# Kernel tuning notes

Hardware: AMD Instinct MI355X
Metric: run time of the kernel (lower is better)

Reference implementation:

```python
import jax, jax.numpy as jnp
import numpy as np

GROUP_SIZE = 128
TOP_K = 2
ZERO_POINT = 8  # Marlin symmetric zero point: w = scale * (q - 8)


def _dequant_int4(q, scales, group_size):
    # q: [E, N, K] int values in [0,15]; scales: [E, N, K//group_size]
    s = jnp.repeat(scales, group_size, axis=-1)  # [E, N, K]
    return (q.astype(jnp.float32) - float(ZERO_POINT)) * s


def setup_inputs() -> dict:
    key = jax.random.key(0)
    k1, k2, k3, k4, k5, k6 = jax.random.split(key, 6)
    B, S, H, I, E = 2, 1024, 2048, 1408, 8
    router_logits = jax.random.normal(k1, (B, S, E), dtype=jnp.float32)
    hidden_states = jax.random.normal(k2, (B, S, H), dtype=jnp.float32)
    fc_gate_up_qweights = jax.random.randint(k3, (E, 2 * I, H), 0, 16, dtype=jnp.int32)
    fc_gate_up_scales = jax.random.uniform(k4, (E, 2 * I, H // GROUP_SIZE), dtype=jnp.float32) * 0.02
    fc_down_qweights = jax.random.randint(k5, (E, H, I), 0, 16, dtype=jnp.int32)
    fc_down_scales = jax.random.uniform(k6, (E, H, I // GROUP_SIZE), dtype=jnp.float32) * 0.02
    return {
        "router_logits": router_logits,
        "hidden_states": hidden_states,
        "fc_gate_up_qweights": fc_gate_up_qweights,
        "fc_gate_up_scales": fc_gate_up_scales,
        "fc_down_qweights": fc_down_qweights,
        "fc_down_scales": fc_down_scales,
    }


def reference(router_logits, hidden_states, fc_gate_up_qweights, fc_gate_up_scales,
              fc_down_qweights, fc_down_scales):
    B, S, H = hidden_states.shape
    E = router_logits.shape[-1]
    T = B * S
    x = hidden_states.reshape(T, H)
    logits = router_logits.reshape(T, E)

    # top-k routing with softmax over selected logits
    top_vals, top_idx = jax.lax.top_k(logits, TOP_K)          # [T, k]
    top_w = jax.nn.softmax(top_vals, axis=-1)                 # [T, k]
    route_w = jnp.zeros((T, E), x.dtype).at[jnp.arange(T)[:, None], top_idx].set(top_w)  # [T, E]

    # dequantize int4 weights: scale * (q - 8), per-group along K
    w_gate_up = _dequant_int4(fc_gate_up_qweights, fc_gate_up_scales, GROUP_SIZE)  # [E, 2I, H]
    w_down = _dequant_int4(fc_down_qweights, fc_down_scales, GROUP_SIZE)          # [E, H, I]

    # grouped GEMM (dense over experts, masked by routing weights)
    gu = jnp.einsum('th,enh->ten', x, w_gate_up)              # [T, E, 2I]
    gate, up = jnp.split(gu, 2, axis=-1)
    act = jax.nn.silu(gate) * up                              # SwiGLU, [T, E, I]
    out = jnp.einsum('tei,ehi,te->th', act, w_down, route_w)  # [T, H]
    return out.reshape(B, S, H)
```

## Files before the change

kernel.cpp:

```cpp
#include <hip/hip_runtime.h>
#include <hip/hip_bf16.h>

#define T_TOKENS 2048
#define H_DIM    2048
#define I_DIM    1408
#define E_NUM    8

typedef __bf16 bf16;
typedef __attribute__((ext_vector_type(8))) __bf16  bf16x8;
typedef __attribute__((ext_vector_type(4))) float   floatx4;

static const size_t OFF_COUNTS = 0;
static const size_t OFF_LISTS  = 256;
static const size_t OFF_WLISTS = OFF_LISTS + (size_t)T_TOKENS * E_NUM * 4;
static const size_t OFF_XB     = 131328;
static const size_t OFF_ACT    = OFF_XB + (size_t)T_TOKENS * H_DIM * 2;
static const size_t OFF_GUPK   = OFF_ACT + (size_t)2 * T_TOKENS * I_DIM * 2;
static const size_t OFF_DNPK   = OFF_GUPK + (size_t)E_NUM * 22 * 32 * 16384;
static const size_t OFF_TMP    = OFF_GUPK;

__device__ __forceinline__ void gload_lds16(const bf16* g, bf16* l)
{
    __builtin_amdgcn_global_load_lds((const __attribute__((address_space(1))) void*)g,
                                     (__attribute__((address_space(3))) void*)l,
                                     16, 0, 0);
}

__global__ __launch_bounds__(256) void pack_gu_kernel(const int* __restrict__ q,
                                                      const float* __restrict__ sc,
                                                      bf16* __restrict__ out)
{
    const int bid = blockIdx.x;
    const int kt  = bid & 31;
    const int en  = bid >> 5;
    const int nt  = en % 22;
    const int e   = en / 22;
    const int tid = threadIdx.x;
    bf16x8* ob = reinterpret_cast<bf16x8*>(out) + (size_t)bid * 1024;
    #pragma unroll
    for (int j = 0; j < 4; ++j) {
        const int s     = tid + 256 * j;
        const int r     = s >> 3;
        const int gl    = (s & 7) ^ (r & 7);
        const int p2    = r >> 4;
        const int is_up = p2 & 1;
        const int icol  = nt * 64 + (p2 >> 1) * 16 + (r & 15);
        const size_t row_q = (size_t)e * 2816 + (is_up ? I_DIM : 0) + icol;
        const int4* qp = reinterpret_cast<const int4*>(q + row_q * H_DIM + kt * 64 + gl * 8);
        int4 a = qp[0], c = qp[1];
        float sv = sc[row_q * 16 + (kt >> 1)];
        float m8 = -8.f * sv;
        bf16x8 bv;
        bv[0] = (bf16)fmaf((float)a.x, sv, m8);
        bv[1] = (bf16)fmaf((float)a.y, sv, m8);
        bv[2] = (bf16)fmaf((float)a.z, sv, m8);
        bv[3] = (bf16)fmaf((float)a.w, sv, m8);
        bv[4] = (bf16)fmaf((float)c.x, sv, m8);
        bv[5] = (bf16)fmaf((float)c.y, sv, m8);
        bv[6] = (bf16)fmaf((float)c.z, sv, m8);
        bv[7] = (bf16)fmaf((float)c.w, sv, m8);
        ob[s] = bv;
    }
}

__global__ __launch_bounds__(256) void pack_dn_kernel(const int* __restrict__ q,
                                                      const float* __restrict__ sc,
                                                      bf16* __restrict__ out)
{
    const int bid = blockIdx.x;
    const int kt  = bid % 22;
    const int en  = bid / 22;
    const int nt  = en & 15;
    const int e   = en >> 4;
    const int tid = threadIdx.x;
    bf16x8* ob = reinterpret_cast<bf16x8*>(out) + (size_t)bid * 1024;
    #pragma unroll
    for (int j = 0; j < 4; ++j) {
        const int s  = tid + 256 * j;
        const int r  = s >> 3;
        const int gl = (s & 7) ^ (r & 7);
        const size_t row_q = (size_t)e * 2048 + nt * 128 + r;
        const int4* qp = reinterpret_cast<const int4*>(q + row_q * I_DIM + kt * 64 + gl * 8);
        int4 a = qp[0], c = qp[1];
        float sv = sc[row_q * 11 + (kt >> 1)];
        float m8 = -8.f * sv;
        bf16x8 bv;
        bv[0] = (bf16)fmaf((float)a.x, sv, m8);
        bv[1] = (bf16)fmaf((float)a.y, sv, m8);
        bv[2] = (bf16)fmaf((float)a.z, sv, m8);
        bv[3] = (bf16)fmaf((float)a.w, sv, m8);
        bv[4] = (bf16)fmaf((float)c.x, sv, m8);
        bv[5] = (bf16)fmaf((float)c.y, sv, m8);
        bv[6] = (bf16)fmaf((float)c.z, sv, m8);
        bv[7] = (bf16)fmaf((float)c.w, sv, m8);
        ob[s] = bv;
    }
}

__global__ void xconv_kernel(const float* __restrict__ x, bf16* __restrict__ xb)
{
    int i = blockIdx.x * blockDim.x + threadIdx.x;
    const float4* x4 = reinterpret_cast<const float4*>(x) + (size_t)i * 2;
    float4 v0 = x4[0], v1 = x4[1];
    bf16x8 bv;
    bv[0] = (bf16)v0.x; bv[1] = (bf16)v0.y; bv[2] = (bf16)v0.z; bv[3] = (bf16)v0.w;
    bv[4] = (bf16)v1.x; bv[5] = (bf16)v1.y; bv[6] = (bf16)v1.z; bv[7] = (bf16)v1.w;
    *reinterpret_cast<bf16x8*>(xb + (size_t)i * 8) = bv;
}

__global__ void router_kernel(const float* __restrict__ logits,
                              int* __restrict__ counts,
                              int* __restrict__ lists,
                              float* __restrict__ wlists)
{
    int t = blockIdx.x * blockDim.x + threadIdx.x;
    if (t >= T_TOKENS) return;
    const float* l = logits + (size_t)t * E_NUM;
    float v0 = -1e30f, v1 = -1e30f;
    int i0 = 0, i1 = 0;
    #pragma unroll
    for (int e = 0; e < E_NUM; ++e) {
        float v = l[e];
        if (v > v0) { v1 = v0; i1 = i0; v0 = v; i0 = e; }
        else if (v > v1) { v1 = v; i1 = e; }
    }
    float w0 = 1.f / (1.f + __expf(v1 - v0));
    float w1 = 1.f - w0;
    int p0 = atomicAdd(&counts[i0], 1);
    lists[i0 * T_TOKENS + p0] = t * 2 + 0;
    wlists[i0 * T_TOKENS + p0] = w0;
    int p1 = atomicAdd(&counts[i1], 1);
    lists[i1 * T_TOKENS + p1] = t * 2 + 1;
    wlists[i1 * T_TOKENS + p1] = w1;
}

__global__ __launch_bounds__(256) void gemm1_kernel(
    const bf16* __restrict__ xb,
    const bf16* __restrict__ wpk,
    const int*  __restrict__ counts,
    const int*  __restrict__ lists,
    bf16*       __restrict__ act)
{
    const int lid = (blockIdx.x & 7) * 352 + (blockIdx.x >> 3);
    const int e   = lid / 352;
    const int r_  = lid - e * 352;
    const int nt  = r_ >> 4;
    const int m0  = (r_ & 15) * 128;
    const int cnt = counts[e];
    if (m0 >= cnt) return;

    __shared__ __align__(16) bf16 Al[8192];
    __shared__ __align__(16) bf16 Bl[8192];
    __shared__ int meta[128];

    const int tid = threadIdx.x;
    if (tid < 128) {
        int m = m0 + tid;
        meta[tid] = lists[e * T_TOKENS + (m < cnt ? m : 0)];
    }
    __syncthreads();

    const int lane = tid & 63;
    const int wv = tid >> 6;
    const int wm = wv >> 1, wn = wv & 1;

    size_t agbl[4];
    #pragma unroll
    for (int j = 0; j < 4; ++j) {
        int g = tid + 256 * j;
        int arow = g >> 3, cg = g & 7;
        agbl[j] = (size_t)(meta[arow] >> 1) * H_DIM + ((cg ^ (arow & 7)) * 8);
    }
    const bf16* bt = wpk + ((size_t)e * 22 + nt) * (32 * 8192) + tid * 8;

    int afr[2][4], bfr[2][4];
    #pragma unroll
    for (int ks = 0; ks < 2; ++ks) {
        int gidx = ks * 4 + (lane >> 4);
        #pragma unroll
        for (int t4 = 0; t4 < 4; ++t4) {
            int ra = wm * 64 + t4 * 16 + (lane & 15);
            afr[ks][t4] = ra * 64 + ((gidx ^ (ra & 7)) * 8);
            int rb = wn * 64 + t4 * 16 + (lane & 15);
            bfr[ks][t4] = rb * 64 + ((gidx ^ (rb & 7)) * 8);
        }
    }

    floatx4 acc[4][4];
    #pragma unroll
    for (int i = 0; i < 4; ++i)
        #pragma unroll
        for (int j = 0; j < 4; ++j)
            acc[i][j] = (floatx4){0.f, 0.f, 0.f, 0.f};

    for (int k0 = 0; k0 < H_DIM; k0 += 64) {
        #pragma unroll
        for (int j = 0; j < 4; ++j)
            gload_lds16(xb + agbl[j] + k0, &Al[(tid + 256 * j) * 8]);
        const bf16* bsrc = bt + (size_t)(k0 >> 6) * 8192;
        #pragma unroll
        for (int j = 0; j < 4; ++j)
            gload_lds16(bsrc + j * 2048, &Bl[tid * 8 + j * 2048]);
        __syncthreads();
        #pragma unroll
        for (int ks = 0; ks < 2; ++ks) {
            bf16x8 af[4], bff[4];
            #pragma unroll
            for (int mt = 0; mt < 4; ++mt)
                af[mt] = *reinterpret_cast<const bf16x8*>(&Al[afr[ks][mt]]);
            #pragma unroll
            for (int ntf = 0; ntf < 4; ++ntf)
                bff[ntf] = *reinterpret_cast<const bf16x8*>(&Bl[bfr[ks][ntf]]);
            #pragma unroll
            for (int mt = 0; mt < 4; ++mt)
                #pragma unroll
                for (int ntf = 0; ntf < 4; ++ntf)
                    acc[mt][ntf] = __builtin_amdgcn_mfma_f32_16x16x32_bf16(af[mt], bff[ntf], acc[mt][ntf], 0, 0, 0);
        }
        __syncthreads();
    }

    const int rbase = (lane >> 4) * 4;
    const int cn = lane & 15;
    #pragma unroll
    for (int mt = 0; mt < 4; ++mt) {
        #pragma unroll
        for (int j = 0; j < 2; ++j) {
            floatx4 g = acc[mt][2 * j];
            floatx4 u = acc[mt][2 * j + 1];
            int col = nt * 64 + (wn * 2 + j) * 16 + cn;
            #pragma unroll
            for (int r = 0; r < 4; ++r) {
                int lrow = wm * 64 + mt * 16 + rbase + r;
                if (m0 + lrow < cnt) {
                    float gate = g[r], up = u[r];
                    float a = gate / (1.f + __expf(-gate)) * up;
                    act[(size_t)meta[lrow] * I_DIM + col] = (bf16)a;
                }
            }
        }
    }
}

__global__ __launch_bounds__(256) void gemm2_kernel(
    const bf16*  __restrict__ act,
    const bf16*  __restrict__ wpk,
    const int*   __restrict__ counts,
    const int*   __restrict__ lists,
    const float* __restrict__ wlists,
    float*       __restrict__ tmp)
{
    const int lid = (blockIdx.x & 7) * 256 + (blockIdx.x >> 3);
    const int e   = lid >> 8;
    const int r_  = lid & 255;
    const int nt  = r_ >> 4;
    const int m0  = (r_ & 15) * 128;
    const int cnt = counts[e];
    if (m0 >= cnt) return;

    __shared__ __align__(16) bf16 Al[8192];
    __shared__ __align__(16) bf16 Bl[8192];
    __shared__ int   meta[128];
    __shared__ float wmeta[128];

    const int tid = threadIdx.x;
    if (tid < 128) {
        int m = m0 + tid;
        int mm = (m < cnt) ? m : 0;
        meta[tid]  = lists[e * T_TOKENS + mm];
        wmeta[tid] = wlists[e * T_TOKENS + mm];
    }
    __syncthreads();

    const int lane = tid & 63;
    const int wv = tid >> 6;
    const int wm = wv >> 1, wn = wv & 1;

    size_t agbl[4];
    #pragma unroll
    for (int j = 0; j < 4; ++j) {
        int g = tid + 256 * j;
        int arow = g >> 3, cg = g & 7;
        agbl[j] = (size_t)meta[arow] * I_DIM + ((cg ^ (arow & 7)) * 8);
    }
    const bf16* bt = wpk + ((size_t)e * 16 + nt) * (22 * 8192) + tid * 8;

    int afr[2][4], bfr[2][4];
    #pragma unroll
    for (int ks = 0; ks < 2; ++ks) {
        int gidx = ks * 4 + (lane >> 4);
        #pragma unroll
        for (int t4 = 0; t4 < 4; ++t4) {
            int ra = wm * 64 + t4 * 16 + (lane & 15);
            afr[ks][t4] = ra * 64 + ((gidx ^ (ra & 7)) * 8);
            int rb = wn * 64 + t4 * 16 + (lane & 15);
            bfr[ks][t4] = rb * 64 + ((gidx ^ (rb & 7)) * 8);
        }
    }

    floatx4 acc[4][4];
    #pragma unroll
    for (int i = 0; i < 4; ++i)
        #pragma unroll
        for (int j = 0; j < 4; ++j)
            acc[i][j] = (floatx4){0.f, 0.f, 0.f, 0.f};

    for (int kt = 0; kt < 22; ++kt) {
        #pragma unroll
        for (int j = 0; j < 4; ++j)
            gload_lds16(act + agbl[j] + kt * 64, &Al[(tid + 256 * j) * 8]);
        const bf16* bsrc = bt + (size_t)kt * 8192;
        #pragma unroll
        for (int j = 0; j < 4; ++j)
            gload_lds16(bsrc + j * 2048, &Bl[tid * 8 + j * 2048]);
        __syncthreads();
        #pragma unroll
        for (int ks = 0; ks < 2; ++ks) {
            bf16x8 af[4], bff[4];
            #pragma unroll
            for (int mt = 0; mt < 4; ++mt)
                af[mt] = *reinterpret_cast<const bf16x8*>(&Al[afr[ks][mt]]);
            #pragma unroll
            for (int ntf = 0; ntf < 4; ++ntf)
                bff[ntf] = *reinterpret_cast<const bf16x8*>(&Bl[bfr[ks][ntf]]);
            #pragma unroll
            for (int mt = 0; mt < 4; ++mt)
                #pragma unroll
                for (int ntf = 0; ntf < 4; ++ntf)
                    acc[mt][ntf] = __builtin_amdgcn_mfma_f32_16x16x32_bf16(af[mt], bff[ntf], acc[mt][ntf], 0, 0, 0);
        }
        __syncthreads();
    }

    const int rbase = (lane >> 4) * 4;
    const int cn = lane & 15;
    #pragma unroll
    for (int mt = 0; mt < 4; ++mt) {
        #pragma unroll
        for (int ntf = 0; ntf < 4; ++ntf) {
            floatx4 v = acc[mt][ntf];
            int col = nt * 128 + wn * 64 + ntf * 16 + cn;
            #pragma unroll
            for (int r = 0; r < 4; ++r) {
                int lrow = wm * 64 + mt * 16 + rbase + r;
                if (m0 + lrow < cnt) {
                    tmp[(size_t)meta[lrow] * H_DIM + col] = wmeta[lrow] * v[r];
                }
            }
        }
    }
}

__global__ void finalize_kernel(const float* __restrict__ tmp, float* __restrict__ out)
{
    int i4 = blockIdx.x * blockDim.x + threadIdx.x;
    int t  = i4 >> 9;
    int h  = (i4 & 511) * 4;
    float4 a = *reinterpret_cast<const float4*>(tmp + ((size_t)2 * t) * H_DIM + h);
    float4 b = *reinterpret_cast<const float4*>(tmp + ((size_t)(2 * t + 1)) * H_DIM + h);
    float4 o;
    o.x = a.x + b.x; o.y = a.y + b.y; o.z = a.z + b.z; o.w = a.w + b.w;
    *reinterpret_cast<float4*>(out + (size_t)t * H_DIM + h) = o;
}

extern "C" void kernel_launch(void* const* d_in, const int* in_sizes, int n_in,
                              void* d_out, int out_size, void* d_ws, size_t ws_size,
                              hipStream_t stream)
{
    const float* router_logits = (const float*)d_in[0];
    const float* x             = (const float*)d_in[1];
    const int*   gu_q          = (const int*)d_in[2];
    const float* gu_s          = (const float*)d_in[3];
    const int*   dn_q          = (const int*)d_in[4];
    const float* dn_s          = (const float*)d_in[5];
    float* out = (float*)d_out;

    char* ws = (char*)d_ws;
    int*   counts = (int*)(ws + OFF_COUNTS);
    int*   lists  = (int*)(ws + OFF_LISTS);
    float* wlists = (float*)(ws + OFF_WLISTS);
    bf16*  xb     = (bf16*)(ws + OFF_XB);
    bf16*  act    = (bf16*)(ws + OFF_ACT);
    bf16*  gu_pk  = (bf16*)(ws + OFF_GUPK);
    bf16*  dn_pk  = (bf16*)(ws + OFF_DNPK);
    float* tmp    = (float*)(ws + OFF_TMP);

    hipMemsetAsync(counts, 0, E_NUM * sizeof(int), stream);

    pack_gu_kernel<<<E_NUM * 22 * 32, 256, 0, stream>>>(gu_q, gu_s, gu_pk);
    pack_dn_kernel<<<E_NUM * 16 * 22, 256, 0, stream>>>(dn_q, dn_s, dn_pk);
    xconv_kernel<<<T_TOKENS * H_DIM / 8 / 256, 256, 0, stream>>>(x, xb);
    router_kernel<<<T_TOKENS / 256, 256, 0, stream>>>(router_logits, counts, lists, wlists);

    gemm1_kernel<<<22 * 16 * E_NUM, 256, 0, stream>>>(xb, gu_pk, counts, lists, act);
    gemm2_kernel<<<16 * 16 * E_NUM, 256, 0, stream>>>(act, dn_pk, counts, lists, wlists, tmp);
    finalize_kernel<<<4096, 256, 0, stream>>>(tmp, out);
}
```

Baseline: 544.2 us.

## Merge prep kernels and overlap down-proj weight packing with gemm1

Combines the gate/up weight packing, activation bf16 conversion and routing into a single prep kernel selected by block-index range. Moves the down-projection weight packing into the gemm1 launch as extra blocks, so its memory traffic can run alongside the gemm1 tiles, many of which exit early for empty experts. This removes several kernel launches and inter-kernel gaps, but the memory-bound pack blocks now share CUs with the GEMM and can slow it.

New measurement: 510.8 us. 6.1% less time.

```diff
diff --git a/kernel.cpp b/kernel.cpp
--- a/kernel.cpp
+++ b/kernel.cpp
@@ -26,121 +26,123 @@
                                      16, 0, 0);
 }
 
-__global__ __launch_bounds__(256) void pack_gu_kernel(const int* __restrict__ q,
-                                                      const float* __restrict__ sc,
-                                                      bf16* __restrict__ out)
+__global__ __launch_bounds__(256) void prep_kernel(
+    const int*   __restrict__ gu_q,
+    const float* __restrict__ gu_s,
+    bf16*        __restrict__ gu_pk,
+    const float* __restrict__ x,
+    bf16*        __restrict__ xb,
+    const float* __restrict__ logits,
+    int*         __restrict__ counts,
+    int*         __restrict__ lists,
+    float*       __restrict__ wlists)
 {
     const int bid = blockIdx.x;
-    const int kt  = bid & 31;
-    const int en  = bid >> 5;
-    const int nt  = en % 22;
-    const int e   = en / 22;
     const int tid = threadIdx.x;
-    bf16x8* ob = reinterpret_cast<bf16x8*>(out) + (size_t)bid * 1024;
-    #pragma unroll
-    for (int j = 0; j < 4; ++j) {
-        const int s     = tid + 256 * j;
-        const int r     = s >> 3;
-        const int gl    = (s & 7) ^ (r & 7);
-        const int p2    = r >> 4;
-        const int is_up = p2 & 1;
-        const int icol  = nt * 64 + (p2 >> 1) * 16 + (r & 15);
-        const size_t row_q = (size_t)e * 2816 + (is_up ? I_DIM : 0) + icol;
-        const int4* qp = reinterpret_cast<const int4*>(q + row_q * H_DIM + kt * 64 + gl * 8);
-        int4 a = qp[0], c = qp[1];
-        float sv = sc[row_q * 16 + (kt >> 1)];
-        float m8 = -8.f * sv;
+
+    if (bid < 5632) {
+        const int kt  = bid & 31;
+        const int en  = bid >> 5;
+        const int nt  = en % 22;
+        const int e   = en / 22;
+        bf16x8* ob = reinterpret_cast<bf16x8*>(gu_pk) + (size_t)bid * 1024;
+        #pragma unroll
+        for (int j = 0; j < 4; ++j) {
+            const int s     = tid + 256 * j;
+            const int r     = s >> 3;
+            const int gl    = (s & 7) ^ (r & 7);
+            const int p2    = r >> 4;
+            const int is_up = p2 & 1;
+            const int icol  = nt * 64 + (p2 >> 1) * 16 + (r & 15);
+            const size_t row_q = (size_t)e * 2816 + (is_up ? I_DIM : 0) + icol;
+            const int4* qp = reinterpret_cast<const int4*>(gu_q + row_q * H_DIM + kt * 64 + gl * 8);
+            int4 a = qp[0], c = qp[1];
+            float sv = gu_s[row_q * 16 + (kt >> 1)];
+            float m8 = -8.f * sv;
+            bf16x8 bv;
+            bv[0] = (bf16)fmaf((float)a.x, sv, m8);
+            bv[1] = (bf16)fmaf((float)a.y, sv, m8);
+            bv[2] = (bf16)fmaf((float)a.z, sv, m8);
+            bv[3] = (bf16)fmaf((float)a.w, sv, m8);
+            bv[4] = (bf16)fmaf((float)c.x, sv, m8);
+            bv[5] = (bf16)fmaf((float)c.y, sv, m8);
+            bv[6] = (bf16)fmaf((float)c.z, sv, m8);
+            bv[7] = (bf16)fmaf((float)c.w, sv, m8);
+            ob[s] = bv;
+        }
+    } else if (bid < 5632 + 2048) {
+        const int i = (bid - 5632) * 256 + tid;
+        const float4* x4 = reinterpret_cast<const float4*>(x) + (size_t)i * 2;
+        float4 v0 = x4[0], v1 = x4[1];
         bf16x8 bv;
-        bv[0] = (bf16)fmaf((float)a.x, sv, m8);
-        bv[1] = (bf16)fmaf((float)a.y, sv, m8);
-        bv[2] = (bf16)fmaf((float)a.z, sv, m8);
-        bv[3] = (bf16)fmaf((float)a.w, sv, m8);
-        bv[4] = (bf16)fmaf((float)c.x, sv, m8);
-        bv[5] = (bf16)fmaf((float)c.y, sv, m8);
-        bv[6] = (bf16)fmaf((float)c.z, sv, m8);
-        bv[7] = (bf16)fmaf((float)c.w, sv, m8);
-        ob[s] = bv;
-    }
-}
-
-__global__ __launch_bounds__(256) void pack_dn_kernel(const int* __restrict__ q,
-                                                      const float* __restrict__ sc,
-                                                      bf16* __restrict__ out)
-{
-    const int bid = blockIdx.x;
-    const int kt  = bid % 22;
-    const int en  = bid / 22;
-    const int nt  = en & 15;
-    const int e   = en >> 4;
+        bv[0] = (bf16)v0.x; bv[1] = (bf16)v0.y; bv[2] = (bf16)v0.z; bv[3] = (bf16)v0.w;
+        bv[4] = (bf16)v1.x; bv[5] = (bf16)v1.y; bv[6] = (bf16)v1.z; bv[7] = (bf16)v1.w;
+        *reinterpret_cast<bf16x8*>(xb + (size_t)i * 8) = bv;
+    } else {
+        const int t = (bid - 7680) * 256 + tid;
+        const float* l = logits + (size_t)t * E_NUM;
+        float v0 = -1e30f, v1 = -1e30f;
+        int i0 = 0, i1 = 0;
+        #pragma unroll
+        for (int e = 0; e < E_NUM; ++e) {
+            float v = l[e];
+            if (v > v0) { v1 = v0; i1 = i0; v0 = v; i0 = e; }
+            else if (v > v1) { v1 = v; i1 = e; }
+        }
+        float w0 = 1.f / (1.f + __expf(v1 - v0));
+        float w1 = 1.f - w0;
+        int p0 = atomicAdd(&counts[i0], 1);
+        lists[i0 * T_TOKENS + p0] = t * 2 + 0;
+        wlists[i0 * T_TOKENS + p0] = w0;
+        int p1 = atomicAdd(&counts[i1], 1);
+        lists[i1 * T_TOKENS + p1] = t * 2 + 1;
+        wlists[i1 * T_TOKENS + p1] = w1;
+    }
+}
+
+__global__ __launch_bounds__(256) void gemm1_packdn_kernel(
+    const bf16*  __restrict__ xb,
+    const bf16*  __restrict__ wpk,
+    const int*   __restrict__ counts,
+    const int*   __restrict__ lists,
+    bf16*        __restrict__ act,
+    const int*   __restrict__ dn_q,
+    const float* __restrict__ dn_s,
+    bf16*        __restrict__ dn_pk)
+{
     const int tid = threadIdx.x;
-    bf16x8* ob = reinterpret_cast<bf16x8*>(out) + (size_t)bid * 1024;
-    #pragma unroll
-    for (int j = 0; j < 4; ++j) {
-        const int s  = tid + 256 * j;
-        const int r  = s >> 3;
-        const int gl = (s & 7) ^ (r & 7);
-        const size_t row_q = (size_t)e * 2048 + nt * 128 + r;
-        const int4* qp = reinterpret_cast<const int4*>(q + row_q * I_DIM + kt * 64 + gl * 8);
-        int4 a = qp[0], c = qp[1];
-        float sv = sc[row_q * 11 + (kt >> 1)];
-        float m8 = -8.f * sv;
-        bf16x8 bv;
-        bv[0] = (bf16)fmaf((float)a.x, sv, m8);
-        bv[1] = (bf16)fmaf((float)a.y, sv, m8);
-        bv[2] = (bf16)fmaf((float)a.z, sv, m8);
-        bv[3] = (bf16)fmaf((float)a.w, sv, m8);
-        bv[4] = (bf16)fmaf((float)c.x, sv, m8);
-        bv[5] = (bf16)fmaf((float)c.y, sv, m8);
-        bv[6] = (bf16)fmaf((float)c.z, sv, m8);
-        bv[7] = (bf16)fmaf((float)c.w, sv, m8);
-        ob[s] = bv;
-    }
-}
-
-__global__ void xconv_kernel(const float* __restrict__ x, bf16* __restrict__ xb)
-{
-    int i = blockIdx.x * blockDim.x + threadIdx.x;
-    const float4* x4 = reinterpret_cast<const float4*>(x) + (size_t)i * 2;
-    float4 v0 = x4[0], v1 = x4[1];
-    bf16x8 bv;
-    bv[0] = (bf16)v0.x; bv[1] = (bf16)v0.y; bv[2] = (bf16)v0.z; bv[3] = (bf16)v0.w;
-    bv[4] = (bf16)v1.x; bv[5] = (bf16)v1.y; bv[6] = (bf16)v1.z; bv[7] = (bf16)v1.w;
-    *reinterpret_cast<bf16x8*>(xb + (size_t)i * 8) = bv;
-}
-
-__global__ void router_kernel(const float* __restrict__ logits,
-                              int* __restrict__ counts,
-                              int* __restrict__ lists,
-                              float* __restrict__ wlists)
-{
-    int t = blockIdx.x * blockDim.x + threadIdx.x;
-    if (t >= T_TOKENS) return;
-    const float* l = logits + (size_t)t * E_NUM;
-    float v0 = -1e30f, v1 = -1e30f;
-    int i0 = 0, i1 = 0;
-    #pragma unroll
-    for (int e = 0; e < E_NUM; ++e) {
-        float v = l[e];
-        if (v > v0) { v1 = v0; i1 = i0; v0 = v; i0 = e; }
-        else if (v > v1) { v1 = v; i1 = e; }
-    }
-    float w0 = 1.f / (1.f + __expf(v1 - v0));
-    float w1 = 1.f - w0;
-    int p0 = atomicAdd(&counts[i0], 1);
-    lists[i0 * T_TOKENS + p0] = t * 2 + 0;
-    wlists[i0 * T_TOKENS + p0] = w0;
-    int p1 = atomicAdd(&counts[i1], 1);
-    lists[i1 * T_TOKENS + p1] = t * 2 + 1;
-    wlists[i1 * T_TOKENS + p1] = w1;
-}
-
-__global__ __launch_bounds__(256) void gemm1_kernel(
-    const bf16* __restrict__ xb,
-    const bf16* __restrict__ wpk,
-    const int*  __restrict__ counts,
-    const int*  __restrict__ lists,
-    bf16*       __restrict__ act)
-{
+
+    if (blockIdx.x >= 2816) {
+        const int pbid = blockIdx.x - 2816;
+        const int kt  = pbid % 22;
+        const int en  = pbid / 22;
+        const int nt  = en & 15;
+        const int e   = en >> 4;
+        bf16x8* ob = reinterpret_cast<bf16x8*>(dn_pk) + (size_t)pbid * 1024;
+        #pragma unroll
+        for (int j = 0; j < 4; ++j) {
+            const int s  = tid + 256 * j;
+            const int r  = s >> 3;
+            const int gl = (s & 7) ^ (r & 7);
+            const size_t row_q = (size_t)e * 2048 + nt * 128 + r;
+            const int4* qp = reinterpret_cast<const int4*>(dn_q + row_q * I_DIM + kt * 64 + gl * 8);
+            int4 a = qp[0], c = qp[1];
+            float sv = dn_s[row_q * 11 + (kt >> 1)];
+            float m8 = -8.f * sv;
+            bf16x8 bv;
+            bv[0] = (bf16)fmaf((float)a.x, sv, m8);
+            bv[1] = (bf16)fmaf((float)a.y, sv, m8);
+            bv[2] = (bf16)fmaf((float)a.z, sv, m8);
+            bv[3] = (bf16)fmaf((float)a.w, sv, m8);
+            bv[4] = (bf16)fmaf((float)c.x, sv, m8);
+            bv[5] = (bf16)fmaf((float)c.y, sv, m8);
+            bv[6] = (bf16)fmaf((float)c.z, sv, m8);
+            bv[7] = (bf16)fmaf((float)c.w, sv, m8);
+            ob[s] = bv;
+        }
+        return;
+    }
+
     const int lid = (blockIdx.x & 7) * 352 + (blockIdx.x >> 3);
     const int e   = lid / 352;
     const int r_  = lid - e * 352;
@@ -153,7 +155,6 @@
     __shared__ __align__(16) bf16 Bl[8192];
     __shared__ int meta[128];
 
-    const int tid = threadIdx.x;
     if (tid < 128) {
         int m = m0 + tid;
         meta[tid] = lists[e * T_TOKENS + (m < cnt ? m : 0)];
@@ -387,12 +388,10 @@
 
     hipMemsetAsync(counts, 0, E_NUM * sizeof(int), stream);
 
-    pack_gu_kernel<<<E_NUM * 22 * 32, 256, 0, stream>>>(gu_q, gu_s, gu_pk);
-    pack_dn_kernel<<<E_NUM * 16 * 22, 256, 0, stream>>>(dn_q, dn_s, dn_pk);
-    xconv_kernel<<<T_TOKENS * H_DIM / 8 / 256, 256, 0, stream>>>(x, xb);
-    router_kernel<<<T_TOKENS / 256, 256, 0, stream>>>(router_logits, counts, lists, wlists);
-
-    gemm1_kernel<<<22 * 16 * E_NUM, 256, 0, stream>>>(xb, gu_pk, counts, lists, act);
+    prep_kernel<<<7688, 256, 0, stream>>>(gu_q, gu_s, gu_pk, x, xb,
+                                          router_logits, counts, lists, wlists);
+    gemm1_packdn_kernel<<<5632, 256, 0, stream>>>(xb, gu_pk, counts, lists, act,
+                                                  dn_q, dn_s, dn_pk);
     gemm2_kernel<<<16 * 16 * E_NUM, 256, 0, stream>>>(act, dn_pk, counts, lists, wlists, tmp);
     finalize_kernel<<<4096, 256, 0, stream>>>(tmp, out);
 }
```
